# Kernel tuning notes

Hardware: AMD Instinct MI355X
Metric: run time of the kernel (lower is better)

## Reference

```python
import jax, jax.numpy as jnp
import numpy as np

EPS = 0.01
N_NODES = 12288
D_PLUS_1 = 65  # 64-dim position + 1 mass
N_EDGES = 262144


def setup_inputs() -> dict:
    key = jax.random.key(0)
    k1, k2 = jax.random.split(key)
    z = jax.random.normal(k1, (N_NODES, D_PLUS_1), dtype=jnp.float32)
    l = jnp.ones((1,), dtype=jnp.float32)  # learnable gravity exponent, init 1.0
    edge_label_index = jax.random.randint(k2, (2, N_EDGES), 0, N_NODES, dtype=jnp.int64)
    return {"z": z, "l": l, "edge_label_index": edge_label_index}


def _multiclass_probs(logits_uv, logits_vu):
    s_uv = jax.nn.sigmoid(logits_uv)
    s_vu = jax.nn.sigmoid(logits_vu)
    p_nb = (1.0 - s_uv) * (1.0 - s_vu)
    p_pu = s_uv * (1.0 - s_vu)
    p_pb = s_uv * s_vu
    p_nu = (1.0 - s_uv) * s_vu
    return jnp.stack([p_nb, p_pu, p_pb, p_nu], axis=1)  # [E, 4]


def reference(z, l, edge_label_index):
    # Full pairwise log-squared-distance logits (as the original decode_all does).
    m = z[:, -1]          # [N] masses
    r = z[:, :-1]         # [N, d] positions
    norm = jnp.sum(r * r, axis=1, keepdims=True)          # [N, 1]
    r2 = norm - 2.0 * (r @ r.T) + norm.T                  # [N, N] squared distances
    logr2 = jnp.log(r2 + EPS)                             # CLAMP is None -> no clamp
    # adj[i, j] = m_j - l * log(||r_i - r_j||^2 + EPS)
    adj = m[None, :] - l * logr2                          # [N, N]
    u = edge_label_index[0]
    v = edge_label_index[1]
    logit_uv = adj[u, v]
    logit_vu = adj[v, u]
    return _multiclass_probs(logit_uv, logit_vu)          # sigmoid=True -> probs [E, 4]
```

## Files before the change

### kernel.cpp

```cpp
#include <hip/hip_runtime.h>


constexpr int kNodes = 12288;
constexpr int kD     = 64;
constexpr int kRow   = 65;
constexpr int kEdges = 262144;
constexpr float kEps = 0.01f;

__global__ __launch_bounds__(256) void edge_kernel(
    const float* __restrict__ z,
    const float* __restrict__ lptr,
    const int*   __restrict__ eidx,
    float4*      __restrict__ out)
{
    const float l = lptr[0];
    const int tid = blockIdx.x * blockDim.x + threadIdx.x;
    const int sub = tid & 15;
    const int estride = (gridDim.x * blockDim.x) >> 4;

    for (int e = tid >> 4; e < kEdges; e += estride) {
        const int u = eidx[e];
        const int v = eidx[kEdges + e];
        const float* zu = z + (long)u * kRow + sub * 4;
        const float* zv = z + (long)v * kRow + sub * 4;

        float p = 0.f;
#pragma unroll
        for (int j = 0; j < 4; ++j) {
            const float d = zu[j] - zv[j];
            p = fmaf(d, d, p);
        }
        p += __shfl_xor(p, 1);
        p += __shfl_xor(p, 2);
        p += __shfl_xor(p, 4);
        p += __shfl_xor(p, 8);

        if (sub == 0) {
            const float logd     = __logf(p + kEps);
            const float logit_uv = z[(long)v * kRow + kD] - l * logd;
            const float logit_vu = z[(long)u * kRow + kD] - l * logd;
            const float suv = 1.f / (1.f + __expf(-logit_uv));
            const float svu = 1.f / (1.f + __expf(-logit_vu));
            out[e] = make_float4((1.f - suv) * (1.f - svu),
                                 suv         * (1.f - svu),
                                 suv         * svu,
                                 (1.f - suv) * svu);
        }
    }
}

extern "C" void kernel_launch(void* const* d_in, const int* in_sizes, int n_in,
                              void* d_out, int out_size, void* d_ws, size_t ws_size,
                              hipStream_t stream) {
    const float* z    = (const float*)d_in[0];
    const float* lptr = (const float*)d_in[1];
    const int*   eidx = (const int*)d_in[2];
    float4*      out  = (float4*)d_out;

    edge_kernel<<<dim3(4096), dim3(256), 0, stream>>>(z, lptr, eidx, out);
}
```

Before: 72.95 us.

## Repack z into aligned 64-float rows and batch four edges per thread group

Adds a repack kernel that copies positions into a 256-byte-aligned [N,64] array and masses into a separate array. The edge kernel can then use float4 vector gathers. Each 16-lane group now processes four edges, issuing all index and row loads up front to raise memory-level parallelism. The cost is an extra kernel launch plus a full pass over z (about 3 MB) on every call, and the kernel now assumes the grid exactly covers the edges.

Result: slower. 75.09 us (+2.9%).

```diff
diff --git a/kernel.cpp b/kernel.cpp
--- a/kernel.cpp
+++ b/kernel.cpp
@@ -7,29 +7,59 @@
 constexpr int kEdges = 262144;
 constexpr float kEps = 0.01f;
 
+__global__ __launch_bounds__(256) void repack_kernel(
+    const float* __restrict__ z,
+    float*       __restrict__ rp,
+    float*       __restrict__ ma)
+{
+    const int f = blockIdx.x * 256 + threadIdx.x;
+    const int n = f / kRow;
+    const int d = f - n * kRow;
+    const float val = z[f];
+    if (d == kD) ma[n] = val;
+    else         rp[(n << 6) + d] = val;
+}
+
 __global__ __launch_bounds__(256) void edge_kernel(
-    const float* __restrict__ z,
+    const float* __restrict__ rp,
+    const float* __restrict__ ma,
     const float* __restrict__ lptr,
     const int*   __restrict__ eidx,
     float4*      __restrict__ out)
 {
     const float l = lptr[0];
-    const int tid = blockIdx.x * blockDim.x + threadIdx.x;
+    const int tid = blockIdx.x * 256 + threadIdx.x;
     const int sub = tid & 15;
-    const int estride = (gridDim.x * blockDim.x) >> 4;
+    const int g   = tid >> 4;
+    constexpr int kStride = 65536;
 
-    for (int e = tid >> 4; e < kEdges; e += estride) {
-        const int u = eidx[e];
-        const int v = eidx[kEdges + e];
-        const float* zu = z + (long)u * kRow + sub * 4;
-        const float* zv = z + (long)v * kRow + sub * 4;
+    int u[4], v[4];
+#pragma unroll
+    for (int i = 0; i < 4; ++i) {
+        u[i] = eidx[g + i * kStride];
+        v[i] = eidx[kEdges + g + i * kStride];
+    }
 
-        float p = 0.f;
+    float4 au[4], av[4];
+    float  mu[4], mv[4];
 #pragma unroll
-        for (int j = 0; j < 4; ++j) {
-            const float d = zu[j] - zv[j];
-            p = fmaf(d, d, p);
-        }
+    for (int i = 0; i < 4; ++i) {
+        au[i] = *reinterpret_cast<const float4*>(rp + (u[i] << 6) + (sub << 2));
+        av[i] = *reinterpret_cast<const float4*>(rp + (v[i] << 6) + (sub << 2));
+        mu[i] = ma[u[i]];
+        mv[i] = ma[v[i]];
+    }
+
+#pragma unroll
+    for (int i = 0; i < 4; ++i) {
+        const float d0 = au[i].x - av[i].x;
+        const float d1 = au[i].y - av[i].y;
+        const float d2 = au[i].z - av[i].z;
+        const float d3 = au[i].w - av[i].w;
+        float p = d0 * d0;
+        p = fmaf(d1, d1, p);
+        p = fmaf(d2, d2, p);
+        p = fmaf(d3, d3, p);
         p += __shfl_xor(p, 1);
         p += __shfl_xor(p, 2);
         p += __shfl_xor(p, 4);
@@ -37,14 +67,15 @@
 
         if (sub == 0) {
             const float logd     = __logf(p + kEps);
-            const float logit_uv = z[(long)v * kRow + kD] - l * logd;
-            const float logit_vu = z[(long)u * kRow + kD] - l * logd;
+            const float logit_uv = mv[i] - l * logd;
+            const float logit_vu = mu[i] - l * logd;
             const float suv = 1.f / (1.f + __expf(-logit_uv));
             const float svu = 1.f / (1.f + __expf(-logit_vu));
-            out[e] = make_float4((1.f - suv) * (1.f - svu),
-                                 suv         * (1.f - svu),
-                                 suv         * svu,
-                                 (1.f - suv) * svu);
+            out[g + i * kStride] = make_float4(
+                (1.f - suv) * (1.f - svu),
+                suv         * (1.f - svu),
+                suv         * svu,
+                (1.f - suv) * svu);
         }
     }
 }
@@ -57,5 +88,9 @@
     const int*   eidx = (const int*)d_in[2];
     float4*      out  = (float4*)d_out;
 
-    edge_kernel<<<dim3(4096), dim3(256), 0, stream>>>(z, lptr, eidx, out);
+    float* rp = (float*)d_ws;
+    float* ma = (float*)d_ws + kNodes * kD;
+
+    repack_kernel<<<dim3((kNodes * kRow) / 256), dim3(256), 0, stream>>>(z, rp, ma);
+    edge_kernel<<<dim3(4096), dim3(256), 0, stream>>>(rp, ma, lptr, eidx, out);
 }
```
